# Kernel optimization log

Hardware: AMD Instinct MI355X
Metric: run time of the kernel (lower is better)

Reference implementation:

```python
import jax, jax.numpy as jnp
import numpy as np

N_NODES = 50000
N_EDGES = 1600000
N_GRAPHS = 2048
DIM = 133
EPS = 1e-5


def gcn_conv(x, W, b, row, col, n_nodes):
    # PyG GCNConv: h = x @ W; add self-loops; sym-normalized scatter-add; + b
    h = x @ W  # [N, D]
    loops = jnp.arange(n_nodes, dtype=row.dtype)
    r = jnp.concatenate([row, loops])
    c = jnp.concatenate([col, loops])
    deg = jax.ops.segment_sum(jnp.ones_like(c, dtype=h.dtype), c, num_segments=n_nodes)
    dinv = jnp.where(deg > 0, jax.lax.rsqrt(deg), 0.0)
    norm = dinv[r] * dinv[c]  # [E+N]
    msg = h[r] * norm[:, None]  # gather + scale
    out = jax.ops.segment_sum(msg, c, num_segments=n_nodes)
    return out + b


def batchnorm_eval(x, gamma, beta, rm, rv):
    return (x - rm) * jax.lax.rsqrt(rv + EPS) * gamma + beta


def setup_inputs() -> dict:
    key = jax.random.key(0)
    ks = jax.random.split(key, 8)
    x = jax.random.normal(ks[0], (N_NODES, DIM), dtype=jnp.float32)
    edge_index = jax.random.randint(ks[1], (2, N_EDGES), 0, N_NODES, dtype=jnp.int64)
    batch = jnp.sort(jax.random.randint(ks[2], (N_NODES,), 0, N_GRAPHS, dtype=jnp.int64))
    s = 1.0 / np.sqrt(DIM)
    W1 = jax.random.uniform(ks[3], (DIM, DIM), jnp.float32, -s, s)
    W2 = jax.random.uniform(ks[4], (DIM, DIM), jnp.float32, -s, s)
    b1 = jnp.zeros((DIM,), jnp.float32)
    b2 = jnp.zeros((DIM,), jnp.float32)
    g1 = jnp.ones((DIM,), jnp.float32); beta1 = jnp.zeros((DIM,), jnp.float32)
    rm1 = jax.random.normal(ks[5], (DIM,), jnp.float32) * 0.1
    rv1 = jnp.ones((DIM,), jnp.float32)
    g2 = jnp.ones((DIM,), jnp.float32); beta2 = jnp.zeros((DIM,), jnp.float32)
    rm2 = jax.random.normal(ks[6], (DIM,), jnp.float32) * 0.1
    rv2 = jnp.ones((DIM,), jnp.float32)
    return {"x": x, "edge_index": edge_index, "batch": batch,
            "W1": W1, "b1": b1, "W2": W2, "b2": b2,
            "g1": g1, "beta1": beta1, "rm1": rm1, "rv1": rv1,
            "g2": g2, "beta2": beta2, "rm2": rm2, "rv2": rv2}


def reference(x, edge_index, batch, W1, b1, W2, b2,
              g1, beta1, rm1, rv1, g2, beta2, rm2, rv2):
    row, col = edge_index[0], edge_index[1]
    h = gcn_conv(x, W1, b1, row, col, N_NODES)
    h = jax.nn.relu(h)
    h = batchnorm_eval(h, g1, beta1, rm1, rv1)  # eval-mode BN; dropout is identity in eval
    h = gcn_conv(h, W2, b2, row, col, N_NODES)
    h = jax.nn.relu(h)
    h = batchnorm_eval(h, g2, beta2, rm2, rv2)
    # global mean pool per graph
    sums = jax.ops.segment_sum(h, batch, num_segments=N_GRAPHS)
    cnts = jax.ops.segment_sum(jnp.ones((N_NODES,), h.dtype), batch, num_segments=N_GRAPHS)
    return sums / jnp.maximum(cnts, 1.0)[:, None]
```

## Files before the change

kernel.cpp:

```cpp
#include <hip/hip_runtime.h>

#define N_NODES  50000
#define N_ROWS   50048
#define N_EDGES  1600000
#define N_GRAPHS 2048
#define DIM      133
#define HMSTR    128
#define HTSTR    8
#define YSTR     160
#define EPSV     1e-5f
#define NRANGE   16
#define RSPAN    3125
#define NSLICE   64
#define BUCKCAP  110000
#define EPB      1563
#define NPN      4

typedef __attribute__((ext_vector_type(8))) short bf16x8;
typedef __attribute__((ext_vector_type(4))) float f32x4;

__device__ __forceinline__ float blo(unsigned u) { return __uint_as_float(u << 16); }
__device__ __forceinline__ float bhi(unsigned u) { return __uint_as_float(u & 0xFFFF0000u); }
__device__ __forceinline__ unsigned short f2bf(float x) {
    unsigned v = __float_as_uint(x);
    return (unsigned short)((v + 0x7FFFu + ((v >> 16) & 1u)) >> 16);
}
__device__ __forceinline__ unsigned packbf(float a, float b) {
    return (unsigned)f2bf(a) | ((unsigned)f2bf(b) << 16);
}


__device__ __forceinline__ void w2bf_one(const float* __restrict__ W,
                                         unsigned short* __restrict__ Wbf, int idx)
{
    int j    = idx & 7;
    int lane = (idx >> 3) & 63;
    int kc   = (idx >> 9) % 5;
    int t    = idx / (8 * 64 * 5);
    int k = kc * 32 + (lane >> 4) * 8 + j;
    int n = t * 16 + (lane & 15);
    float v = (k < DIM && n < DIM) ? W[k * DIM + n] : 0.f;
    Wbf[idx] = f2bf(v);
}

#define PRB_X 15625
#define PRB_W 189
#define PRB_Z 1064

__global__ __launch_bounds__(256) void k_prep(const float* __restrict__ x,
                                              unsigned* __restrict__ Abf,
                                              const float* __restrict__ W1,
                                              const float* __restrict__ W2,
                                              unsigned short* __restrict__ Wbf1,
                                              unsigned short* __restrict__ Wbf2,
                                              const int* __restrict__ batch,
                                              float* __restrict__ inv_cnt,
                                              int* __restrict__ bcnt,
                                              float* __restrict__ outp)
{
    int b = blockIdx.x;
    if (b < PRB_X) {
        int idx = b * 256 + threadIdx.x;
        if (idx >= N_NODES * 80) return;
        int r  = idx / 80;
        int c2 = (idx - r * 80) * 2;
        float a = (c2     < DIM) ? x[(size_t)r * DIM + c2]     : 0.f;
        float bb = (c2 + 1 < DIM) ? x[(size_t)r * DIM + c2 + 1] : 0.f;
        Abf[idx] = packbf(a, bb);
        return;
    }
    if (b < PRB_X + PRB_W) {
        int tid = (b - PRB_X) * 256 + threadIdx.x;
        if (tid < 23040) {
            w2bf_one(W1, Wbf1, tid);
        } else if (tid < 46080) {
            w2bf_one(W2, Wbf2, tid - 23040);
        } else if (tid < 46080 + N_GRAPHS) {
            int g = tid - 46080;
            int a0 = 0, b0 = N_NODES;
            while (a0 < b0) { int m = (a0 + b0) >> 1; if (batch[m] < g) a0 = m + 1; else b0 = m; }
            int a1 = a0, b1 = N_NODES;
            while (a1 < b1) { int m = (a1 + b1) >> 1; if (batch[m] < g + 1) a1 = m + 1; else b1 = m; }
            inv_cnt[g] = 1.0f / (float)max(a1 - a0, 1);
        } else if (tid < 46080 + N_GRAPHS + NRANGE) {
            bcnt[tid - 46080 - N_GRAPHS] = 0;
        }
        return;
    }
    int i = (b - PRB_X - PRB_W) * 256 + threadIdx.x;
    outp[i] = 0.f;
}


__global__ __launch_bounds__(256) void k_part(const int* __restrict__ row,
                                              const int* __restrict__ col,
                                              int* __restrict__ bcnt,
                                              unsigned* __restrict__ buckets)
{
    __shared__ int cnt[NRANGE];
    __shared__ int cur[NRANGE];
    int e0 = blockIdx.x * EPB;
    if (threadIdx.x < NRANGE) cnt[threadIdx.x] = 0;
    __syncthreads();
    int e1 = min(e0 + EPB, N_EDGES);
    for (int e = e0 + threadIdx.x; e < e1; e += 256)
        atomicAdd(&cnt[col[e] / RSPAN], 1);
    __syncthreads();
    if (threadIdx.x < NRANGE)
        cur[threadIdx.x] = atomicAdd(&bcnt[threadIdx.x], cnt[threadIdx.x]);
    __syncthreads();
    for (int e = e0 + threadIdx.x; e < e1; e += 256) {
        int c = col[e];
        int r = c / RSPAN;
        int p = atomicAdd(&cur[r], 1);
        buckets[(size_t)r * BUCKCAP + p] =
            ((unsigned)row[e] << 12) | (unsigned)(c - r * RSPAN);
    }
}

__global__ __launch_bounds__(256) void k_count2(const unsigned* __restrict__ buckets,
                                                const int* __restrict__ bcnt,
                                                int* __restrict__ deg2)
{
    __shared__ int hist[RSPAN];
    int r = blockIdx.x & (NRANGE - 1);
    int s = blockIdx.x >> 4;
    int lo = r * RSPAN;
    for (int i = threadIdx.x; i < RSPAN; i += 256) hist[i] = 0;
    __syncthreads();
    int n = bcnt[r];
    int chunk = (n + NSLICE - 1) / NSLICE;
    int e0 = s * chunk, e1 = min(e0 + chunk, n);
    const unsigned* b = buckets + (size_t)r * BUCKCAP;
    for (int e = e0 + threadIdx.x; e < e1; e += 256)
        atomicAdd(&hist[b[e] & 0xFFFu], 1);
    __syncthreads();
    for (int i = threadIdx.x; i < RSPAN; i += 256)
        deg2[(size_t)s * N_NODES + lo + i] = hist[i];
}

__global__ __launch_bounds__(256) void k_scan1(const int* __restrict__ deg2,
                                               float* __restrict__ dinv,
                                               int* __restrict__ offs,
                                               int* __restrict__ bsum)
{
    __shared__ int sd[256];
    int t = threadIdx.x;
    int idx = blockIdx.x * 256 + t;
    int v = 0;
    if (idx < N_NODES) {
        for (int s = 0; s < NSLICE; s++) v += deg2[(size_t)s * N_NODES + idx];
        dinv[idx] = rsqrtf((float)v + 1.0f);
    }
    sd[t] = v; __syncthreads();
    for (int o = 1; o < 256; o <<= 1) {
        int add = (t >= o) ? sd[t - o] : 0;
        __syncthreads();
        sd[t] += add;
        __syncthreads();
    }
    if (idx < N_NODES) offs[idx] = sd[t] - v;
    if (t == 255) bsum[blockIdx.x] = sd[255];
}

__global__ __launch_bounds__(256) void k_scan23C(int* __restrict__ offs,
                                                 const int* __restrict__ bsum,
                                                 int* __restrict__ deg2, int nb)
{
    __shared__ int sd[256];
    int t = threadIdx.x;
    int v = (t < nb) ? bsum[t] : 0;
    sd[t] = v; __syncthreads();
    for (int o = 1; o < 256; o <<= 1) {
        int add = (t >= o) ? sd[t - o] : 0;
        __syncthreads();
        sd[t] += add;
        __syncthreads();
    }
    int boff = sd[blockIdx.x] - bsum[blockIdx.x];
    int idx = blockIdx.x * 256 + t;
    if (idx < N_NODES) {
        int off = offs[idx] + boff;
        offs[idx] = off;
        int run = off;
        for (int s = 0; s < NSLICE; s++) {
            int d = deg2[(size_t)s * N_NODES + idx];
            deg2[(size_t)s * N_NODES + idx] = run;
            run += d;
        }
    } else if (idx == N_NODES) {
        offs[N_NODES] = N_EDGES;
    }
}

__global__ __launch_bounds__(256) void k_fill2(const unsigned* __restrict__ buckets,
                                               const int* __restrict__ bcnt,
                                               const int* __restrict__ offs2,
                                               const float* __restrict__ dinv,
                                               unsigned* __restrict__ csr)
{
    __shared__ int cur[RSPAN];
    int r = blockIdx.x & (NRANGE - 1);
    int s = blockIdx.x >> 4;
    int lo = r * RSPAN;
    for (int i = threadIdx.x; i < RSPAN; i += 256)
        cur[i] = offs2[(size_t)s * N_NODES + lo + i];
    __syncthreads();
    int n = bcnt[r];
    int chunk = (n + NSLICE - 1) / NSLICE;
    int e0 = s * chunk, e1 = min(e0 + chunk, n);
    const unsigned* b = buckets + (size_t)r * BUCKCAP;
    for (int e = e0 + threadIdx.x; e < e1; e += 256) {
        unsigned v = b[e];
        int src = (int)(v >> 12);
        int p = atomicAdd(&cur[v & 0xFFFu], 1);
        csr[p] = ((unsigned)src << 16) | (unsigned)f2bf(dinv[src]);
    }
}

__global__ __launch_bounds__(256) void k_gemm_mfma(const unsigned short* __restrict__ A,
                                                   const unsigned short* __restrict__ Wbf,
                                                   unsigned short* __restrict__ Hmain,
                                                   unsigned short* __restrict__ Htail, int M)
{
    int wave = threadIdx.x >> 6, lane = threadIdx.x & 63;
    int quad = lane >> 4, l16 = lane & 15;
    int m = blockIdx.x * 64 + wave * 16 + l16;

    const bf16x8* Arow = (const bf16x8*)(A + (size_t)m * YSTR);
    const bf16x8* Bq   = (const bf16x8*)Wbf;

    f32x4 acc[9] = {};
#pragma unroll
    for (int kc = 0; kc < 5; kc++) {
        bf16x8 af = Arow[kc * 4 + quad];
#pragma unroll
        for (int t = 0; t < 9; t++) {
            bf16x8 bfr = Bq[(t * 5 + kc) * 64 + lane];
            acc[t] = __builtin_amdgcn_mfma_f32_16x16x32_bf16(af, bfr, acc[t], 0, 0, 0);
        }
    }

    int gr0 = blockIdx.x * 64 + wave * 16 + quad * 4;
#pragma unroll
    for (int t = 0; t < 9; t++) {
        int c = t * 16 + l16;
#pragma unroll
        for (int reg = 0; reg < 4; reg++) {
            int gr = gr0 + reg;
            if (gr < M) {
                if (c < HMSTR) {
                    Hmain[(size_t)gr * HMSTR + c] = f2bf(acc[t][reg]);
                } else if (c < HMSTR + HTSTR) {
                    float v = (c < DIM) ? acc[t][reg] : 0.f;
                    Htail[(size_t)gr * HTSTR + (c - HMSTR)] = f2bf(v);
                }
            }
        }
    }
}


__device__ __forceinline__ void agg_row(const unsigned short* __restrict__ hmain,
                                        const unsigned short* __restrict__ htail,
                                        const int* __restrict__ offs,
                                        const unsigned* __restrict__ csr,
                                        const float* __restrict__ dinv,
                                        const float* __restrict__ bias,
                                        const float* __restrict__ gam,
                                        const float* __restrict__ bet,
                                        const float* __restrict__ rmean,
                                        const float* __restrict__ rvar,
                                        int node, int lane, int l2,
                                        float& va, float& vb, float& ta, float& tb)
{
    const unsigned* hm = (const unsigned*)hmain;
    const unsigned* ht = (const unsigned*)htail;

    float di = dinv[node];
    unsigned pw0 = hm[((size_t)node << 6) + lane];
    unsigned pw1 = ht[((unsigned)node << 2) + l2];
    float2 a0; a0.x = di * blo(pw0); a0.y = di * bhi(pw0);
    float2 a1; a1.x = di * blo(pw1); a1.y = di * bhi(pw1);

    int s0 = offs[node], s1 = offs[node + 1];
    int e = s0;
    for (; e + 8 <= s1; e += 8) {
        unsigned rec[8];
#pragma unroll
        for (int u = 0; u < 8; u++)
            rec[u] = __builtin_amdgcn_readfirstlane(csr[e + u]);
        unsigned q0[8], q1[8];
#pragma unroll
        for (int u = 0; u < 8; u++) {
            const unsigned* hr = hm + ((size_t)(rec[u] >> 16) << 6);
            const unsigned* tr = ht + ((rec[u] >> 16) << 2);
            q0[u] = hr[lane];
            q1[u] = tr[l2];
        }
#pragma unroll
        for (int u = 0; u < 8; u++) {
            float w = __uint_as_float(rec[u] << 16);
            a0.x += w * blo(q0[u]); a0.y += w * bhi(q0[u]);
            a1.x += w * blo(q1[u]); a1.y += w * bhi(q1[u]);
        }
    }
    for (; e < s1; e++) {
        unsigned rec = __builtin_amdgcn_readfirstlane(csr[e]);
        const unsigned* hr = hm + ((size_t)(rec >> 16) << 6);
        const unsigned* tr = ht + ((rec >> 16) << 2);
        float w = __uint_as_float(rec << 16);
        unsigned q0 = hr[lane];
        unsigned q1 = tr[l2];
        a0.x += w * blo(q0); a0.y += w * bhi(q0);
        a1.x += w * blo(q1); a1.y += w * bhi(q1);
    }

    {
        int c = 2 * lane;
        float v = di * a0.x + bias[c];
        v = fmaxf(v, 0.f);
        va = (v - rmean[c]) * (gam[c] * rsqrtf(rvar[c] + EPSV)) + bet[c];
        int c1 = c + 1;
        v = di * a0.y + bias[c1];
        v = fmaxf(v, 0.f);
        vb = (v - rmean[c1]) * (gam[c1] * rsqrtf(rvar[c1] + EPSV)) + bet[c1];
    }
    ta = 0.f; tb = 0.f;
    if (lane < 4) {
        int c = 128 + 2 * l2;
        if (c < DIM) {
            float v = di * a1.x + bias[c];
            v = fmaxf(v, 0.f);
            ta = (v - rmean[c]) * (gam[c] * rsqrtf(rvar[c] + EPSV)) + bet[c];
        }
        int c1 = c + 1;
        if (c1 < DIM) {
            float v = di * a1.y + bias[c1];
            v = fmaxf(v, 0.f);
            tb = (v - rmean[c1]) * (gam[c1] * rsqrtf(rvar[c1] + EPSV)) + bet[c1];
        }
    }
}

template <bool FINAL>
__global__ __launch_bounds__(256) void k_agg(const unsigned short* __restrict__ hmain,
                                             const unsigned short* __restrict__ htail,
                                             const int* __restrict__ offs,
                                             const unsigned* __restrict__ csr,
                                             const float* __restrict__ dinv,
                                             const float* __restrict__ bias,
                                             const float* __restrict__ gam,
                                             const float* __restrict__ bet,
                                             const float* __restrict__ rmean,
                                             const float* __restrict__ rvar,
                                             unsigned short* __restrict__ y,
                                             const int* __restrict__ batch,
                                             const float* __restrict__ inv_cnt,
                                             float* __restrict__ outp)
{
    int lane = threadIdx.x & 63;
    int l2 = lane & 3;

    if (!FINAL) {
        int node = __builtin_amdgcn_readfirstlane(blockIdx.x * 4 + (threadIdx.x >> 6));
        if (node >= N_NODES) return;
        float va, vb, ta, tb;
        agg_row(hmain, htail, offs, csr, dinv, bias, gam, bet, rmean, rvar,
                node, lane, l2, va, vb, ta, tb);
        ((unsigned*)(y + (size_t)node * YSTR))[lane] = packbf(va, vb);
        if (lane < 16)
            ((unsigned*)(y + (size_t)node * YSTR))[64 + lane] =
                (lane < 4) ? packbf(ta, tb) : 0u;
        return;
    }

    int node0 = __builtin_amdgcn_readfirstlane((blockIdx.x * 4 + (threadIdx.x >> 6)) * NPN);
    if (node0 >= N_NODES) return;
    int nend = min(node0 + NPN, N_NODES);

    float p0x = 0.f, p0y = 0.f, p1x = 0.f, p1y = 0.f;
    int curg = batch[node0];

    for (int node = node0; node < nend; node++) {
        int bg = batch[node];
        if (bg != curg) {
            float ic = inv_cnt[curg];
            int c = 2 * lane;
            atomicAdd(&outp[(size_t)curg * DIM + c],     p0x * ic);
            atomicAdd(&outp[(size_t)curg * DIM + c + 1], p0y * ic);
            if (lane < 4) {
                int ct = 128 + 2 * l2;
                if (ct     < DIM) atomicAdd(&outp[(size_t)curg * DIM + ct],     p1x * ic);
                if (ct + 1 < DIM) atomicAdd(&outp[(size_t)curg * DIM + ct + 1], p1y * ic);
            }
            p0x = p0y = p1x = p1y = 0.f;
            curg = bg;
        }
        float va, vb, ta, tb;
        agg_row(hmain, htail, offs, csr, dinv, bias, gam, bet, rmean, rvar,
                node, lane, l2, va, vb, ta, tb);
        p0x += va; p0y += vb; p1x += ta; p1y += tb;
    }
    {
        float ic = inv_cnt[curg];
        int c = 2 * lane;
        atomicAdd(&outp[(size_t)curg * DIM + c],     p0x * ic);
        atomicAdd(&outp[(size_t)curg * DIM + c + 1], p0y * ic);
        if (lane < 4) {
            int ct = 128 + 2 * l2;
            if (ct     < DIM) atomicAdd(&outp[(size_t)curg * DIM + ct],     p1x * ic);
            if (ct + 1 < DIM) atomicAdd(&outp[(size_t)curg * DIM + ct + 1], p1y * ic);
        }
    }
}


extern "C" void kernel_launch(void* const* d_in, const int* in_sizes, int n_in,
                              void* d_out, int out_size, void* d_ws, size_t ws_size,
                              hipStream_t stream)
{
    const float* x   = (const float*)d_in[0];
    const int*   ei  = (const int*)d_in[1];
    const int*   bat = (const int*)d_in[2];
    const float* W1  = (const float*)d_in[3];
    const float* b1  = (const float*)d_in[4];
    const float* W2  = (const float*)d_in[5];
    const float* b2  = (const float*)d_in[6];
    const float* g1  = (const float*)d_in[7];
    const float* be1 = (const float*)d_in[8];
    const float* rm1 = (const float*)d_in[9];
    const float* rv1 = (const float*)d_in[10];
    const float* g2  = (const float*)d_in[11];
    const float* be2 = (const float*)d_in[12];
    const float* rm2 = (const float*)d_in[13];
    const float* rv2 = (const float*)d_in[14];
    float* outp = (float*)d_out;
    char* ws = (char*)d_ws;

    int*   bcnt    = (int*)  (ws + 0);
    int*   offs    = (int*)  (ws + 200000);
    float* dinv    = (float*)(ws + 400016);
    float* inv_cnt = (float*)(ws + 600016);
    int*   bsum    = (int*)  (ws + 608208);
    unsigned* csr  = (unsigned*)(ws + 610256);
    unsigned short* Wbf1 = (unsigned short*)(ws + 7010256);
    unsigned short* Wbf2 = (unsigned short*)(ws + 7056336);
    unsigned short* Abf  = (unsigned short*)(ws + 7102416);
    unsigned short* Y1   = Abf;
    unsigned short* Hm   = (unsigned short*)(ws + 23118080);
    unsigned short* Ht   = (unsigned short*)(ws + 35930368);
    unsigned* buckets = (unsigned*)(ws + 23118080);
    int*      deg2    = (int*)    (ws + 30158080);

    const int* row = ei;
    const int* col = ei + N_EDGES;

    int nbl = (N_NODES + 255) / 256;

    k_prep  <<<dim3(PRB_X + PRB_W + PRB_Z), dim3(256), 0, stream>>>(
                x, (unsigned*)Abf, W1, W2, Wbf1, Wbf2, bat, inv_cnt, bcnt, outp);
    k_part  <<<dim3(1024), dim3(256), 0, stream>>>(row, col, bcnt, buckets);
    k_count2<<<dim3(NSLICE * NRANGE), dim3(256), 0, stream>>>(buckets, bcnt, deg2);
    k_scan1 <<<dim3(nbl), dim3(256), 0, stream>>>(deg2, dinv, offs, bsum);
    k_scan23C<<<dim3(nbl), dim3(256), 0, stream>>>(offs, bsum, deg2, nbl);
    k_fill2 <<<dim3(NSLICE * NRANGE), dim3(256), 0, stream>>>(buckets, bcnt, deg2, dinv, csr);

    int gbl = N_ROWS / 64;
    k_gemm_mfma<<<dim3(gbl), dim3(256), 0, stream>>>(Abf, Wbf1, Hm, Ht, N_NODES);
    k_agg<false><<<dim3(N_NODES / 4), dim3(256), 0, stream>>>(Hm, Ht, offs, csr, dinv,
                                                              b1, g1, be1, rm1, rv1,
                                                              Y1, nullptr, nullptr, nullptr);
    k_gemm_mfma<<<dim3(gbl), dim3(256), 0, stream>>>(Y1, Wbf2, Hm, Ht, N_NODES);
    int fbl = (N_NODES + 4 * NPN - 1) / (4 * NPN);
    k_agg<true><<<dim3(fbl), dim3(256), 0, stream>>>(Hm, Ht, offs, csr, dinv,
                                                     b2, g2, be2, rm2, rv2,
                                                     nullptr, bat, inv_cnt, outp);
}
```

Baseline: 316.4 us.

## Replace coarse bucket CSR build with fine 512-bucket partition and fused histogram-scan

The CSR construction now partitions edges into 512 fine buckets of 98 destination nodes instead of 16 coarse ranges split across 64 slices. A single per-bucket kernel computes the degree histogram, dinv and offsets (using a prefix over bucket counts), and a fill kernel scatters the edges. This replaces five kernels (count, two scans, fill) with three and drops the 64x-sliced degree array, cutting launches and memory traffic. The cost is that each bucket is processed by only one block, which limits parallelism, and the fixed bucket capacity of 3600 assumes a balanced random column distribution.

```diff
diff --git a/kernel.cpp b/kernel.cpp
--- a/kernel.cpp
+++ b/kernel.cpp
@@ -9,12 +9,13 @@
 #define HTSTR    8
 #define YSTR     160
 #define EPSV     1e-5f
-#define NRANGE   16
-#define RSPAN    3125
-#define NSLICE   64
-#define BUCKCAP  110000
-#define EPB      1563
 #define NPN      4
+
+#define NR2   512
+#define SPAN  98
+#define BCAP2 3600
+#define NPART 256
+#define EPB3  6250
 
 typedef __attribute__((ext_vector_type(8))) short bf16x8;
 typedef __attribute__((ext_vector_type(4))) float f32x4;
@@ -44,7 +45,7 @@
 }
 
 #define PRB_X 15625
-#define PRB_W 189
+#define PRB_W 190
 #define PRB_Z 1064
 
 __global__ __launch_bounds__(256) void k_prep(const float* __restrict__ x,
@@ -82,7 +83,7 @@
             int a1 = a0, b1 = N_NODES;
             while (a1 < b1) { int m = (a1 + b1) >> 1; if (batch[m] < g + 1) a1 = m + 1; else b1 = m; }
             inv_cnt[g] = 1.0f / (float)max(a1 - a0, 1);
-        } else if (tid < 46080 + N_GRAPHS + NRANGE) {
+        } else if (tid < 46080 + N_GRAPHS + NR2) {
             bcnt[tid - 46080 - N_GRAPHS] = 0;
         }
         return;
@@ -97,123 +98,94 @@
                                               int* __restrict__ bcnt,
                                               unsigned* __restrict__ buckets)
 {
-    __shared__ int cnt[NRANGE];
-    __shared__ int cur[NRANGE];
-    int e0 = blockIdx.x * EPB;
-    if (threadIdx.x < NRANGE) cnt[threadIdx.x] = 0;
-    __syncthreads();
-    int e1 = min(e0 + EPB, N_EDGES);
+    __shared__ int cnt[NR2];
+    __shared__ int cur[NR2];
+    for (int i = threadIdx.x; i < NR2; i += 256) cnt[i] = 0;
+    __syncthreads();
+    int e0 = blockIdx.x * EPB3;
+    int e1 = min(e0 + EPB3, N_EDGES);
     for (int e = e0 + threadIdx.x; e < e1; e += 256)
-        atomicAdd(&cnt[col[e] / RSPAN], 1);
-    __syncthreads();
-    if (threadIdx.x < NRANGE)
-        cur[threadIdx.x] = atomicAdd(&bcnt[threadIdx.x], cnt[threadIdx.x]);
+        atomicAdd(&cnt[col[e] / SPAN], 1);
+    __syncthreads();
+    for (int i = threadIdx.x; i < NR2; i += 256) {
+        int c = cnt[i];
+        cur[i] = c ? atomicAdd(&bcnt[i], c) : 0;
+    }
     __syncthreads();
     for (int e = e0 + threadIdx.x; e < e1; e += 256) {
         int c = col[e];
-        int r = c / RSPAN;
+        int r = c / SPAN;
         int p = atomicAdd(&cur[r], 1);
-        buckets[(size_t)r * BUCKCAP + p] =
-            ((unsigned)row[e] << 12) | (unsigned)(c - r * RSPAN);
-    }
-}
-
-__global__ __launch_bounds__(256) void k_count2(const unsigned* __restrict__ buckets,
-                                                const int* __restrict__ bcnt,
-                                                int* __restrict__ deg2)
-{
-    __shared__ int hist[RSPAN];
-    int r = blockIdx.x & (NRANGE - 1);
-    int s = blockIdx.x >> 4;
-    int lo = r * RSPAN;
-    for (int i = threadIdx.x; i < RSPAN; i += 256) hist[i] = 0;
-    __syncthreads();
+        buckets[(size_t)r * BCAP2 + p] =
+            ((unsigned)row[e] << 7) | (unsigned)(c - r * SPAN);
+    }
+}
+
+__global__ __launch_bounds__(256) void k_hist(const unsigned* __restrict__ buckets,
+                                              const int* __restrict__ bcnt,
+                                              float* __restrict__ dinv,
+                                              int* __restrict__ offs)
+{
+    __shared__ int hist[128];
+    __shared__ int rbuf[256];
+    int r = blockIdx.x, t = threadIdx.x;
+
+    if (t < 128) hist[t] = 0;
+    int s = 0;
+    for (int i = t; i < r; i += 256) s += bcnt[i];
+    rbuf[t] = s;
+    __syncthreads();
+    for (int o = 128; o > 0; o >>= 1) {
+        if (t < o) rbuf[t] += rbuf[t + o];
+        __syncthreads();
+    }
+    int rb = rbuf[0];
+    __syncthreads();
+
     int n = bcnt[r];
-    int chunk = (n + NSLICE - 1) / NSLICE;
-    int e0 = s * chunk, e1 = min(e0 + chunk, n);
-    const unsigned* b = buckets + (size_t)r * BUCKCAP;
-    for (int e = e0 + threadIdx.x; e < e1; e += 256)
-        atomicAdd(&hist[b[e] & 0xFFFu], 1);
-    __syncthreads();
-    for (int i = threadIdx.x; i < RSPAN; i += 256)
-        deg2[(size_t)s * N_NODES + lo + i] = hist[i];
-}
-
-__global__ __launch_bounds__(256) void k_scan1(const int* __restrict__ deg2,
-                                               float* __restrict__ dinv,
-                                               int* __restrict__ offs,
-                                               int* __restrict__ bsum)
-{
-    __shared__ int sd[256];
-    int t = threadIdx.x;
-    int idx = blockIdx.x * 256 + t;
-    int v = 0;
-    if (idx < N_NODES) {
-        for (int s = 0; s < NSLICE; s++) v += deg2[(size_t)s * N_NODES + idx];
-        dinv[idx] = rsqrtf((float)v + 1.0f);
-    }
-    sd[t] = v; __syncthreads();
-    for (int o = 1; o < 256; o <<= 1) {
-        int add = (t >= o) ? sd[t - o] : 0;
+    const unsigned* bk = buckets + (size_t)r * BCAP2;
+    for (int e = t; e < n; e += 256)
+        atomicAdd(&hist[bk[e] & 127u], 1);
+    __syncthreads();
+
+    int hv = (t < 128) ? hist[t] : 0;
+    if (t < 128) rbuf[t] = hv;
+    __syncthreads();
+    for (int o = 1; o < 128; o <<= 1) {
+        int add = (t < 128 && t >= o) ? rbuf[t - o] : 0;
         __syncthreads();
-        sd[t] += add;
+        if (t < 128) rbuf[t] += add;
         __syncthreads();
     }
-    if (idx < N_NODES) offs[idx] = sd[t] - v;
-    if (t == 255) bsum[blockIdx.x] = sd[255];
-}
-
-__global__ __launch_bounds__(256) void k_scan23C(int* __restrict__ offs,
-                                                 const int* __restrict__ bsum,
-                                                 int* __restrict__ deg2, int nb)
-{
-    __shared__ int sd[256];
-    int t = threadIdx.x;
-    int v = (t < nb) ? bsum[t] : 0;
-    sd[t] = v; __syncthreads();
-    for (int o = 1; o < 256; o <<= 1) {
-        int add = (t >= o) ? sd[t - o] : 0;
-        __syncthreads();
-        sd[t] += add;
-        __syncthreads();
-    }
-    int boff = sd[blockIdx.x] - bsum[blockIdx.x];
-    int idx = blockIdx.x * 256 + t;
-    if (idx < N_NODES) {
-        int off = offs[idx] + boff;
-        offs[idx] = off;
-        int run = off;
-        for (int s = 0; s < NSLICE; s++) {
-            int d = deg2[(size_t)s * N_NODES + idx];
-            deg2[(size_t)s * N_NODES + idx] = run;
-            run += d;
-        }
-    } else if (idx == N_NODES) {
-        offs[N_NODES] = N_EDGES;
-    }
-}
-
-__global__ __launch_bounds__(256) void k_fill2(const unsigned* __restrict__ buckets,
-                                               const int* __restrict__ bcnt,
-                                               const int* __restrict__ offs2,
-                                               const float* __restrict__ dinv,
-                                               unsigned* __restrict__ csr)
-{
-    __shared__ int cur[RSPAN];
-    int r = blockIdx.x & (NRANGE - 1);
-    int s = blockIdx.x >> 4;
-    int lo = r * RSPAN;
-    for (int i = threadIdx.x; i < RSPAN; i += 256)
-        cur[i] = offs2[(size_t)s * N_NODES + lo + i];
+    if (t < SPAN) {
+        int node = r * SPAN + t;
+        if (node < N_NODES) {
+            dinv[node] = rsqrtf((float)hv + 1.0f);
+            offs[node] = rb + rbuf[t] - hv;
+        }
+    }
+    if (r == 0 && t == 0) offs[N_NODES] = N_EDGES;
+}
+
+__global__ __launch_bounds__(256) void k_fill(const unsigned* __restrict__ buckets,
+                                              const int* __restrict__ bcnt,
+                                              const int* __restrict__ offs,
+                                              const float* __restrict__ dinv,
+                                              unsigned* __restrict__ csr)
+{
+    __shared__ int cur[SPAN];
+    int r = blockIdx.x, t = threadIdx.x;
+    if (t < SPAN) {
+        int node = r * SPAN + t;
+        cur[t] = (node < N_NODES) ? offs[node] : 0;
+    }
     __syncthreads();
     int n = bcnt[r];
-    int chunk = (n + NSLICE - 1) / NSLICE;
-    int e0 = s * chunk, e1 = min(e0 + chunk, n);
-    const unsigned* b = buckets + (size_t)r * BUCKCAP;
-    for (int e = e0 + threadIdx.x; e < e1; e += 256) {
-        unsigned v = b[e];
-        int src = (int)(v >> 12);
-        int p = atomicAdd(&cur[v & 0xFFFu], 1);
+    const unsigned* bk = buckets + (size_t)r * BCAP2;
+    for (int e = t; e < n; e += 256) {
+        unsigned v = bk[e];
+        int src = (int)(v >> 7);
+        int p = atomicAdd(&cur[v & 127u], 1);
         csr[p] = ((unsigned)src << 16) | (unsigned)f2bf(dinv[src]);
     }
 }
@@ -442,7 +414,6 @@
     int*   offs    = (int*)  (ws + 200000);
     float* dinv    = (float*)(ws + 400016);
     float* inv_cnt = (float*)(ws + 600016);
-    int*   bsum    = (int*)  (ws + 608208);
     unsigned* csr  = (unsigned*)(ws + 610256);
     unsigned short* Wbf1 = (unsigned short*)(ws + 7010256);
     unsigned short* Wbf2 = (unsigned short*)(ws + 7056336);
@@ -451,20 +422,15 @@
     unsigned short* Hm   = (unsigned short*)(ws + 23118080);
     unsigned short* Ht   = (unsigned short*)(ws + 35930368);
     unsigned* buckets = (unsigned*)(ws + 23118080);
-    int*      deg2    = (int*)    (ws + 30158080);
 
     const int* row = ei;
     const int* col = ei + N_EDGES;
 
-    int nbl = (N_NODES + 255) / 256;
-
     k_prep  <<<dim3(PRB_X + PRB_W + PRB_Z), dim3(256), 0, stream>>>(
                 x, (unsigned*)Abf, W1, W2, Wbf1, Wbf2, bat, inv_cnt, bcnt, outp);
-    k_part  <<<dim3(1024), dim3(256), 0, stream>>>(row, col, bcnt, buckets);
-    k_count2<<<dim3(NSLICE * NRANGE), dim3(256), 0, stream>>>(buckets, bcnt, deg2);
-    k_scan1 <<<dim3(nbl), dim3(256), 0, stream>>>(deg2, dinv, offs, bsum);
-    k_scan23C<<<dim3(nbl), dim3(256), 0, stream>>>(offs, bsum, deg2, nbl);
-    k_fill2 <<<dim3(NSLICE * NRANGE), dim3(256), 0, stream>>>(buckets, bcnt, deg2, dinv, csr);
+    k_part  <<<dim3(NPART), dim3(256), 0, stream>>>(row, col, bcnt, buckets);
+    k_hist  <<<dim3(NR2),   dim3(256), 0, stream>>>(buckets, bcnt, dinv, offs);
+    k_fill  <<<dim3(NR2),   dim3(256), 0, stream>>>(buckets, bcnt, offs, dinv, csr);
 
     int gbl = N_ROWS / 64;
     k_gemm_mfma<<<dim3(gbl), dim3(256), 0, stream>>>(Abf, Wbf1, Hm, Ht, N_NODES);
```

Result: faster. 306.5 us (-3.1%).
